# Performance work log

Hardware: AMD Instinct MI355X
Metric: run time of the kernel (lower is better)

Reference implementation:

```python
import jax
import jax.numpy as jnp
import numpy as np

IN_FEATS = 784
HIDDEN_DIM = 1024
BATCH = 1024


def setup_inputs() -> dict:
    key = jax.random.key(0)
    k_px, k_W, k_c, k_V, k_b = jax.random.split(key, 5)
    pixels = jax.random.uniform(k_px, (BATCH, IN_FEATS), dtype=jnp.float32)
    W = jax.random.normal(k_W, (HIDDEN_DIM, IN_FEATS), dtype=jnp.float32)
    c = jax.random.normal(k_c, (HIDDEN_DIM,), dtype=jnp.float32)
    V = jax.random.normal(k_V, (IN_FEATS, HIDDEN_DIM), dtype=jnp.float32)
    b = jax.random.normal(k_b, (IN_FEATS,), dtype=jnp.float32)
    return {"pixels": pixels, "W": W, "c": c, "V": V, "b": b}


def reference(pixels, W, c, V, b):
    # pixels: [B, D]; W: [H, D]; c: [H]; V: [D, H]; b: [D]
    B = pixels.shape[0]
    a0 = jnp.broadcast_to(c[None, :], (B, c.shape[0]))  # [B, H]

    def step(a, inp):
        w_col, v_row, b_i, x_i = inp  # [H], [H], [], [B]
        h = jax.nn.sigmoid(a)                     # [B, H]
        pred_i = b_i + h @ v_row                  # [B]
        a_next = a + w_col[None, :] * x_i[:, None]  # rank-1 accumulator update
        return a_next, pred_i

    xs = (W.T, V, b, pixels.T)  # each leading dim D (scan over visible units)
    _, preds = jax.lax.scan(step, a0, xs)  # preds: [D, B]
    return preds.T  # [B, D]
```

## Files before the change

### kernel.cpp

```cpp
#include <hip/hip_runtime.h>
#include <stdint.h>

#define B_ 1024
#define D_ 784
#define H_ 1024
#define BH_ (B_ * H_)
#define LOG2E 1.4426950408889634f


typedef float v2f __attribute__((ext_vector_type(2)));

__device__ __forceinline__ int seg_bound(int s) {
    const int b[5] = {0, 200, 392, 592, 784};
    return b[s];
}

__device__ __forceinline__ size_t vw_idx(int i, int h, int part) {
    return (size_t)i * 2048 + (part * 4 + ((h & 7) >> 1)) * 256
         + ((h & 511) >> 3) * 4 + (h & 1) * 2 + (h >> 9);
}

__global__ __launch_bounds__(256) void prep(const float* __restrict__ V,
                                            const float* __restrict__ W,
                                            const float* __restrict__ px,
                                            float* __restrict__ VWf,
                                            float* __restrict__ G) {
    __shared__ float smem[1056];
    const int t = threadIdx.x;

    if (blockIdx.x < 800) {
        int i0 = (blockIdx.x % 25) * 32;
        int h0 = (blockIdx.x / 25) * 32;
        int tx = t & 31, ty = t >> 5;
#pragma unroll
        for (int j = 0; j < 4; ++j) {
            int i = i0 + ty + j * 8;
            if (i < D_)
                VWf[vw_idx(i, h0 + tx, 0)] = V[(size_t)i * H_ + h0 + tx];
        }
#pragma unroll
        for (int j = 0; j < 4; ++j) {
            int h = h0 + ty + j * 8;
            int i = i0 + tx;
            float v = 0.f;
            if (i < D_) v = W[(size_t)h * D_ + i] * -LOG2E;
            smem[(ty + j * 8) * 33 + tx] = v;
        }
        __syncthreads();
#pragma unroll
        for (int j = 0; j < 4; ++j) {
            int i = i0 + ty + j * 8;
            if (i < D_)
                VWf[vw_idx(i, h0 + tx, 1)] = smem[tx * 33 + ty + j * 8];
        }
    } else {
        float* xs = smem;
        float* ws = smem + 512;
        int idx = blockIdx.x - 800;
        int r   = idx >> 8;
        int b0  = (idx & 15) * 64;
        int h0  = ((idx >> 4) & 15) * 64;
        int j0s = seg_bound(r), j1s = seg_bound(r + 1);

        const int tb = t >> 4, th = t & 15;
        float acc[4][4];
#pragma unroll
        for (int bi = 0; bi < 4; ++bi)
#pragma unroll
            for (int hh = 0; hh < 4; ++hh) acc[bi][hh] = 0.f;

        const int xb = t >> 3;
        const int xj = t & 7;
        const int wh = t >> 1, wj = (t & 1) * 4;

        for (int j0 = j0s; j0 < j1s; j0 += 8) {
            float xv0 = px[(size_t)(b0 + xb) * D_ + j0 + xj];
            float xv1 = px[(size_t)(b0 + 32 + xb) * D_ + j0 + xj];
            float4 wv = make_float4(0, 0, 0, 0);
            if (t < 128) wv = *(const float4*)(W + (size_t)(h0 + wh) * D_ + j0 + wj);
            __syncthreads();
            xs[xj * 64 + xb]      = xv0;
            xs[xj * 64 + 32 + xb] = xv1;
            if (t < 128) {
                ws[(wj + 0) * 64 + wh] = wv.x * LOG2E;
                ws[(wj + 1) * 64 + wh] = wv.y * LOG2E;
                ws[(wj + 2) * 64 + wh] = wv.z * LOG2E;
                ws[(wj + 3) * 64 + wh] = wv.w * LOG2E;
            }
            __syncthreads();
#pragma unroll
            for (int jj = 0; jj < 8; ++jj) {
                float4 xq = *(float4*)&xs[jj * 64 + tb * 4];
                float4 wq = *(float4*)&ws[jj * 64 + th * 4];
                float xa[4] = {xq.x, xq.y, xq.z, xq.w};
                float wa[4] = {wq.x, wq.y, wq.z, wq.w};
#pragma unroll
                for (int bi = 0; bi < 4; ++bi)
#pragma unroll
                    for (int hh = 0; hh < 4; ++hh)
                        acc[bi][hh] = fmaf(xa[bi], wa[hh], acc[bi][hh]);
            }
        }
        float* dst = G + (size_t)r * BH_;
#pragma unroll
        for (int bi = 0; bi < 4; ++bi) {
            float4 o = make_float4(acc[bi][0], acc[bi][1], acc[bi][2], acc[bi][3]);
            *(float4*)(dst + (size_t)(b0 + tb * 4 + bi) * H_ + h0 + th * 4) = o;
        }
    }
}

template <int CTRL>
__device__ __forceinline__ float dpp_add(float p) {
    int s = __builtin_amdgcn_update_dpp(0, __float_as_int(p), CTRL, 0xf, 0xf, true);
    return p + __int_as_float(s);
}
__device__ __forceinline__ float reduce64(float p) {
    p = dpp_add<0x111>(p);
    p = dpp_add<0x112>(p);
    p = dpp_add<0x114>(p);
    p = dpp_add<0x118>(p);
    p = dpp_add<0x142>(p);
    p = dpp_add<0x143>(p);
    return p;
}

__device__ __forceinline__ void tree16(v2f (&An)[8], const float4 (&Va)[4], const float4 (&Wa)[4],
                                       float xi, v2f& n, v2f& d) {
    const v2f* va = (const v2f*)&Va[0];
    const v2f* wa = (const v2f*)&Wa[0];
    const v2f one = {1.f, 1.f};
    const v2f clamp15 = {15.f, 15.f};
    v2f xiv; xiv.x = xi; xiv.y = xi;
    v2f q[8];
#pragma unroll
    for (int k = 0; k < 8; ++k) {
        v2f m = __builtin_elementwise_min(clamp15, An[k]);
        v2f e;
        e.x = __builtin_amdgcn_exp2f(m.x);
        e.y = __builtin_amdgcn_exp2f(m.y);
        q[k] = one + e;
        An[k] = wa[k] * xiv + An[k];
    }
    v2f a01 = va[0] * q[1] + va[1] * q[0];
    v2f a23 = va[2] * q[3] + va[3] * q[2];
    v2f a45 = va[4] * q[5] + va[5] * q[4];
    v2f a67 = va[6] * q[7] + va[7] * q[6];
    v2f q01 = q[0] * q[1], q23 = q[2] * q[3];
    v2f q45 = q[4] * q[5], q67 = q[6] * q[7];
    v2f n0123 = a01 * q23 + a23 * q01;
    v2f n4567 = a45 * q67 + a67 * q45;
    v2f q0123 = q01 * q23, q4567 = q45 * q67;
    d = q0123 * q4567;
    n = n0123 * q4567 + n4567 * q0123;
}

__global__ __launch_bounds__(256, 4) void nade_main(
    const float* __restrict__ px,
    const float* __restrict__ c,
    const float* __restrict__ VWf,
    const float* __restrict__ G,
    const float* __restrict__ bias,
    float* __restrict__ out)
{
    const int lane = threadIdx.x & 63;
    const int wid  = threadIdx.x >> 6;
    const int bid  = blockIdx.x;
    const int s    = (bid >> 1) & 3;
    const int rb   = ((bid >> 3) << 1) | (bid & 1);
    const int row  = rb * 4 + wid;

    const int i0s = seg_bound(s), i1s = seg_bound(s + 1);

    const int hA = lane * 8;
    const int hB = 512 + hA;

    v2f An[8];
    {
        float4 c0 = *(const float4*)(c + hA);
        float4 c1 = *(const float4*)(c + hA + 4);
        float4 c2 = *(const float4*)(c + hB);
        float4 c3 = *(const float4*)(c + hB + 4);
        An[0].x = -c0.x * LOG2E; An[0].y = -c2.x * LOG2E;
        An[1].x = -c0.y * LOG2E; An[1].y = -c2.y * LOG2E;
        An[2].x = -c0.z * LOG2E; An[2].y = -c2.z * LOG2E;
        An[3].x = -c0.w * LOG2E; An[3].y = -c2.w * LOG2E;
        An[4].x = -c1.x * LOG2E; An[4].y = -c3.x * LOG2E;
        An[5].x = -c1.y * LOG2E; An[5].y = -c3.y * LOG2E;
        An[6].x = -c1.z * LOG2E; An[6].y = -c3.z * LOG2E;
        An[7].x = -c1.w * LOG2E; An[7].y = -c3.w * LOG2E;
        for (int r = 0; r < s; ++r) {
            const float* gp = G + (size_t)r * BH_ + (size_t)row * H_;
            float4 g0 = *(const float4*)(gp + hA);
            float4 g1 = *(const float4*)(gp + hA + 4);
            float4 g2 = *(const float4*)(gp + hB);
            float4 g3 = *(const float4*)(gp + hB + 4);
            An[0].x -= g0.x; An[0].y -= g2.x;
            An[1].x -= g0.y; An[1].y -= g2.y;
            An[2].x -= g0.z; An[2].y -= g2.z;
            An[3].x -= g0.w; An[3].y -= g2.w;
            An[4].x -= g1.x; An[4].y -= g3.x;
            An[5].x -= g1.y; An[5].y -= g3.y;
            An[6].x -= g1.z; An[6].y -= g3.z;
            An[7].x -= g1.w; An[7].y -= g3.w;
        }
    }

    const float* xp = px + (size_t)row * D_;
    const float* vp = VWf + (size_t)i0s * 2048 + lane * 4;

    float4 VaC[4], WaC[4];
#pragma unroll
    for (int u = 0; u < 4; ++u) {
        VaC[u] = *(const float4*)(vp + u * 256);
        WaC[u] = *(const float4*)(vp + 1024 + u * 256);
    }
    vp += 2048;
    float4 xq = *(const float4*)(xp + i0s);

    for (int ib = i0s; ib < i1s; ib += 4) {
        int xb = (ib + 4 < i1s) ? (ib + 4) : i0s;
        float4 xq_n = *(const float4*)(xp + xb);
        float xa[4] = {xq.x, xq.y, xq.z, xq.w};
        float pr[4];
#pragma unroll
        for (int j = 0; j < 4; ++j) {
            float4 VaN[4], WaN[4];
#pragma unroll
            for (int u = 0; u < 4; ++u) {
                VaN[u] = *(const float4*)(vp + u * 256);
                WaN[u] = *(const float4*)(vp + 1024 + u * 256);
            }
            vp += 2048;
            v2f n, d;
            tree16(An, VaC, WaC, xa[j], n, d);
            float p = fmaf(n.x, __builtin_amdgcn_rcpf(d.x),
                           n.y * __builtin_amdgcn_rcpf(d.y));
            pr[j] = reduce64(p);
#pragma unroll
            for (int u = 0; u < 4; ++u) { VaC[u] = VaN[u]; WaC[u] = WaN[u]; }
        }
        float4 b4 = *(const float4*)(bias + ib);
        if (lane == 63) {
            float4 o = make_float4(pr[0] + b4.x, pr[1] + b4.y, pr[2] + b4.z, pr[3] + b4.w);
            *(float4*)(out + (size_t)row * D_ + ib) = o;
        }
        xq = xq_n;
    }
}

extern "C" void kernel_launch(void* const* d_in, const int* in_sizes, int n_in,
                              void* d_out, int out_size, void* d_ws, size_t ws_size,
                              hipStream_t stream) {
    const float* px   = (const float*)d_in[0];
    const float* W    = (const float*)d_in[1];
    const float* c    = (const float*)d_in[2];
    const float* V    = (const float*)d_in[3];
    const float* bias = (const float*)d_in[4];
    float* out = (float*)d_out;

    float* VWf = (float*)d_ws;
    float* G   = (float*)((char*)d_ws + (size_t)788 * 8192);

    prep<<<dim3(1568), 256, 0, stream>>>(V, W, px, VWf, G);

    nade_main<<<dim3(1024), 256, 0, stream>>>(px, c, VWf, G, bias, out);
}
```

Before: 317.9 us.

## Fuse prep and main kernels into one cooperative launch with grid sync

Merges the transpose/prep kernel and the partial-GEMM prep into the main NADE kernel. Prep work runs as a grid-stride task loop, followed by a cooperative grid-wide sync before the recurrence phase, which removes one kernel launch and the gap between kernels. The VWf transpose is also rewritten to stage both W and V tiles in shared memory and emit float4 stores. This adds 16.5KB of shared memory per block, which may limit occupancy at 4 blocks/CU, and it relies on a cooperative launch of 1024 blocks being co-resident. If that launch fails, it falls back to two launches.

```diff
diff --git a/kernel.cpp b/kernel.cpp
--- a/kernel.cpp
+++ b/kernel.cpp
@@ -1,5 +1,8 @@
 #include <hip/hip_runtime.h>
+#include <hip/hip_cooperative_groups.h>
 #include <stdint.h>
+
+namespace cg = cooperative_groups;
 
 #define B_ 1024
 #define D_ 784
@@ -13,101 +16,6 @@
 __device__ __forceinline__ int seg_bound(int s) {
     const int b[5] = {0, 200, 392, 592, 784};
     return b[s];
-}
-
-__device__ __forceinline__ size_t vw_idx(int i, int h, int part) {
-    return (size_t)i * 2048 + (part * 4 + ((h & 7) >> 1)) * 256
-         + ((h & 511) >> 3) * 4 + (h & 1) * 2 + (h >> 9);
-}
-
-__global__ __launch_bounds__(256) void prep(const float* __restrict__ V,
-                                            const float* __restrict__ W,
-                                            const float* __restrict__ px,
-                                            float* __restrict__ VWf,
-                                            float* __restrict__ G) {
-    __shared__ float smem[1056];
-    const int t = threadIdx.x;
-
-    if (blockIdx.x < 800) {
-        int i0 = (blockIdx.x % 25) * 32;
-        int h0 = (blockIdx.x / 25) * 32;
-        int tx = t & 31, ty = t >> 5;
-#pragma unroll
-        for (int j = 0; j < 4; ++j) {
-            int i = i0 + ty + j * 8;
-            if (i < D_)
-                VWf[vw_idx(i, h0 + tx, 0)] = V[(size_t)i * H_ + h0 + tx];
-        }
-#pragma unroll
-        for (int j = 0; j < 4; ++j) {
-            int h = h0 + ty + j * 8;
-            int i = i0 + tx;
-            float v = 0.f;
-            if (i < D_) v = W[(size_t)h * D_ + i] * -LOG2E;
-            smem[(ty + j * 8) * 33 + tx] = v;
-        }
-        __syncthreads();
-#pragma unroll
-        for (int j = 0; j < 4; ++j) {
-            int i = i0 + ty + j * 8;
-            if (i < D_)
-                VWf[vw_idx(i, h0 + tx, 1)] = smem[tx * 33 + ty + j * 8];
-        }
-    } else {
-        float* xs = smem;
-        float* ws = smem + 512;
-        int idx = blockIdx.x - 800;
-        int r   = idx >> 8;
-        int b0  = (idx & 15) * 64;
-        int h0  = ((idx >> 4) & 15) * 64;
-        int j0s = seg_bound(r), j1s = seg_bound(r + 1);
-
-        const int tb = t >> 4, th = t & 15;
-        float acc[4][4];
-#pragma unroll
-        for (int bi = 0; bi < 4; ++bi)
-#pragma unroll
-            for (int hh = 0; hh < 4; ++hh) acc[bi][hh] = 0.f;
-
-        const int xb = t >> 3;
-        const int xj = t & 7;
-        const int wh = t >> 1, wj = (t & 1) * 4;
-
-        for (int j0 = j0s; j0 < j1s; j0 += 8) {
-            float xv0 = px[(size_t)(b0 + xb) * D_ + j0 + xj];
-            float xv1 = px[(size_t)(b0 + 32 + xb) * D_ + j0 + xj];
-            float4 wv = make_float4(0, 0, 0, 0);
-            if (t < 128) wv = *(const float4*)(W + (size_t)(h0 + wh) * D_ + j0 + wj);
-            __syncthreads();
-            xs[xj * 64 + xb]      = xv0;
-            xs[xj * 64 + 32 + xb] = xv1;
-            if (t < 128) {
-                ws[(wj + 0) * 64 + wh] = wv.x * LOG2E;
-                ws[(wj + 1) * 64 + wh] = wv.y * LOG2E;
-                ws[(wj + 2) * 64 + wh] = wv.z * LOG2E;
-                ws[(wj + 3) * 64 + wh] = wv.w * LOG2E;
-            }
-            __syncthreads();
-#pragma unroll
-            for (int jj = 0; jj < 8; ++jj) {
-                float4 xq = *(float4*)&xs[jj * 64 + tb * 4];
-                float4 wq = *(float4*)&ws[jj * 64 + th * 4];
-                float xa[4] = {xq.x, xq.y, xq.z, xq.w};
-                float wa[4] = {wq.x, wq.y, wq.z, wq.w};
-#pragma unroll
-                for (int bi = 0; bi < 4; ++bi)
-#pragma unroll
-                    for (int hh = 0; hh < 4; ++hh)
-                        acc[bi][hh] = fmaf(xa[bi], wa[hh], acc[bi][hh]);
-            }
-        }
-        float* dst = G + (size_t)r * BH_;
-#pragma unroll
-        for (int bi = 0; bi < 4; ++bi) {
-            float4 o = make_float4(acc[bi][0], acc[bi][1], acc[bi][2], acc[bi][3]);
-            *(float4*)(dst + (size_t)(b0 + tb * 4 + bi) * H_ + h0 + th * 4) = o;
-        }
-    }
 }
 
 template <int CTRL>
@@ -155,97 +63,217 @@
     n = n0123 * q4567 + n4567 * q0123;
 }
 
-__global__ __launch_bounds__(256, 4) void nade_main(
+__global__ __launch_bounds__(256, 4) void nade_fused(
     const float* __restrict__ px,
+    const float* __restrict__ W,
     const float* __restrict__ c,
-    const float* __restrict__ VWf,
-    const float* __restrict__ G,
+    const float* __restrict__ V,
     const float* __restrict__ bias,
-    float* __restrict__ out)
+    float* __restrict__ VWf,
+    float* __restrict__ G,
+    float* __restrict__ out,
+    int mode)
 {
-    const int lane = threadIdx.x & 63;
-    const int wid  = threadIdx.x >> 6;
-    const int bid  = blockIdx.x;
-    const int s    = (bid >> 1) & 3;
-    const int rb   = ((bid >> 3) << 1) | (bid & 1);
-    const int row  = rb * 4 + wid;
-
-    const int i0s = seg_bound(s), i1s = seg_bound(s + 1);
-
-    const int hA = lane * 8;
-    const int hB = 512 + hA;
-
-    v2f An[8];
+    __shared__ float smem[4224];
+    const int t   = threadIdx.x;
+    const int bid = blockIdx.x;
+
+    if (mode != 1) {
+        for (int task = bid; task < 1168; task += gridDim.x) {
+            __syncthreads();
+            if (task < 768) {
+                float* xs = smem;
+                float* ws = smem + 512;
+                int idx = task;
+                int r   = idx >> 8;
+                int b0  = (idx & 15) * 64;
+                int h0  = ((idx >> 4) & 15) * 64;
+                int j0s = seg_bound(r), j1s = seg_bound(r + 1);
+
+                const int tb = t >> 4, th = t & 15;
+                float acc[4][4];
+#pragma unroll
+                for (int bi = 0; bi < 4; ++bi)
+#pragma unroll
+                    for (int hh = 0; hh < 4; ++hh) acc[bi][hh] = 0.f;
+
+                const int xb = t >> 3;
+                const int xj = t & 7;
+                const int wh = t >> 1, wj = (t & 1) * 4;
+
+                for (int j0 = j0s; j0 < j1s; j0 += 8) {
+                    float xv0 = px[(size_t)(b0 + xb) * D_ + j0 + xj];
+                    float xv1 = px[(size_t)(b0 + 32 + xb) * D_ + j0 + xj];
+                    float4 wv = make_float4(0, 0, 0, 0);
+                    if (t < 128) wv = *(const float4*)(W + (size_t)(h0 + wh) * D_ + j0 + wj);
+                    __syncthreads();
+                    xs[xj * 64 + xb]      = xv0;
+                    xs[xj * 64 + 32 + xb] = xv1;
+                    if (t < 128) {
+                        ws[(wj + 0) * 64 + wh] = wv.x * LOG2E;
+                        ws[(wj + 1) * 64 + wh] = wv.y * LOG2E;
+                        ws[(wj + 2) * 64 + wh] = wv.z * LOG2E;
+                        ws[(wj + 3) * 64 + wh] = wv.w * LOG2E;
+                    }
+                    __syncthreads();
+#pragma unroll
+                    for (int jj = 0; jj < 8; ++jj) {
+                        float4 xq = *(float4*)&xs[jj * 64 + tb * 4];
+                        float4 wq = *(float4*)&ws[jj * 64 + th * 4];
+                        float xa[4] = {xq.x, xq.y, xq.z, xq.w};
+                        float wa[4] = {wq.x, wq.y, wq.z, wq.w};
+#pragma unroll
+                        for (int bi = 0; bi < 4; ++bi)
+#pragma unroll
+                            for (int hh = 0; hh < 4; ++hh)
+                                acc[bi][hh] = fmaf(xa[bi], wa[hh], acc[bi][hh]);
+                    }
+                }
+                float* dst = G + (size_t)r * BH_;
+#pragma unroll
+                for (int bi = 0; bi < 4; ++bi) {
+                    float4 o = make_float4(acc[bi][0], acc[bi][1], acc[bi][2], acc[bi][3]);
+                    *(float4*)(dst + (size_t)(b0 + tb * 4 + bi) * H_ + h0 + th * 4) = o;
+                }
+            } else {
+                int pt = task - 768;
+                int i0 = (pt % 25) * 32;
+                int h0 = (pt / 25) * 32;
+                float* smW = smem;
+                float* smV = smem + 2112;
+                const int tx = t & 31, ty = t >> 5;
+#pragma unroll
+                for (int u = 0; u < 2; ++u)
+#pragma unroll
+                    for (int j = 0; j < 4; ++j) {
+                        int rl = ty + j * 8;
+                        float w = 0.f;
+                        int iw = i0 + tx;
+                        if (iw < D_) w = W[(size_t)(h0 + u * 512 + rl) * D_ + iw] * -LOG2E;
+                        smW[u * 1056 + rl * 33 + tx] = w;
+                        float v = 0.f;
+                        int iv = i0 + rl;
+                        if (iv < D_) v = V[(size_t)iv * H_ + h0 + u * 512 + tx];
+                        smV[u * 1056 + rl * 33 + tx] = v;
+                    }
+                __syncthreads();
+                const int img = t >> 3;
+                const int iw  = i0 + img;
+                if (iw < D_) {
+                    const int sub = t & 7;
+                    const int sp  = sub >> 1;
+                    const int q   = sub & 1;
+                    float vv[8], wv[8];
+#pragma unroll
+                    for (int e = 0; e < 8; ++e) {
+                        int p = q * 8 + e;
+                        int m = p >> 2, par = (p >> 1) & 1, comp = p & 1;
+                        int hl = 8 * m + sp * 2 + par;
+                        wv[e] = smW[comp * 1056 + hl * 33 + img];
+                        vv[e] = smV[comp * 1056 + img * 33 + hl];
+                    }
+                    float* dst = VWf + (size_t)iw * 2048;
+                    int cb = h0 / 2 + q * 8;
+                    *(float4*)(dst + sp * 256 + cb)           = make_float4(vv[0], vv[1], vv[2], vv[3]);
+                    *(float4*)(dst + sp * 256 + cb + 4)       = make_float4(vv[4], vv[5], vv[6], vv[7]);
+                    *(float4*)(dst + (4 + sp) * 256 + cb)     = make_float4(wv[0], wv[1], wv[2], wv[3]);
+                    *(float4*)(dst + (4 + sp) * 256 + cb + 4) = make_float4(wv[4], wv[5], wv[6], wv[7]);
+                }
+            }
+        }
+    }
+
+    if (mode == 2) {
+        __threadfence();
+        cg::this_grid().sync();
+        __threadfence();
+    }
+    if (mode == 0) return;
+
     {
-        float4 c0 = *(const float4*)(c + hA);
-        float4 c1 = *(const float4*)(c + hA + 4);
-        float4 c2 = *(const float4*)(c + hB);
-        float4 c3 = *(const float4*)(c + hB + 4);
-        An[0].x = -c0.x * LOG2E; An[0].y = -c2.x * LOG2E;
-        An[1].x = -c0.y * LOG2E; An[1].y = -c2.y * LOG2E;
-        An[2].x = -c0.z * LOG2E; An[2].y = -c2.z * LOG2E;
-        An[3].x = -c0.w * LOG2E; An[3].y = -c2.w * LOG2E;
-        An[4].x = -c1.x * LOG2E; An[4].y = -c3.x * LOG2E;
-        An[5].x = -c1.y * LOG2E; An[5].y = -c3.y * LOG2E;
-        An[6].x = -c1.z * LOG2E; An[6].y = -c3.z * LOG2E;
-        An[7].x = -c1.w * LOG2E; An[7].y = -c3.w * LOG2E;
-        for (int r = 0; r < s; ++r) {
-            const float* gp = G + (size_t)r * BH_ + (size_t)row * H_;
-            float4 g0 = *(const float4*)(gp + hA);
-            float4 g1 = *(const float4*)(gp + hA + 4);
-            float4 g2 = *(const float4*)(gp + hB);
-            float4 g3 = *(const float4*)(gp + hB + 4);
-            An[0].x -= g0.x; An[0].y -= g2.x;
-            An[1].x -= g0.y; An[1].y -= g2.y;
-            An[2].x -= g0.z; An[2].y -= g2.z;
-            An[3].x -= g0.w; An[3].y -= g2.w;
-            An[4].x -= g1.x; An[4].y -= g3.x;
-            An[5].x -= g1.y; An[5].y -= g3.y;
-            An[6].x -= g1.z; An[6].y -= g3.z;
-            An[7].x -= g1.w; An[7].y -= g3.w;
+        const int lane = t & 63;
+        const int wid  = t >> 6;
+        const int s    = (bid >> 1) & 3;
+        const int rb   = ((bid >> 3) << 1) | (bid & 1);
+        const int row  = rb * 4 + wid;
+
+        const int i0s = seg_bound(s), i1s = seg_bound(s + 1);
+
+        const int hA = lane * 8;
+        const int hB = 512 + hA;
+
+        v2f An[8];
+        {
+            float4 c0 = *(const float4*)(c + hA);
+            float4 c1 = *(const float4*)(c + hA + 4);
+            float4 c2 = *(const float4*)(c + hB);
+            float4 c3 = *(const float4*)(c + hB + 4);
+            An[0].x = -c0.x * LOG2E; An[0].y = -c2.x * LOG2E;
+            An[1].x = -c0.y * LOG2E; An[1].y = -c2.y * LOG2E;
+            An[2].x = -c0.z * LOG2E; An[2].y = -c2.z * LOG2E;
+            An[3].x = -c0.w * LOG2E; An[3].y = -c2.w * LOG2E;
+            An[4].x = -c1.x * LOG2E; An[4].y = -c3.x * LOG2E;
+            An[5].x = -c1.y * LOG2E; An[5].y = -c3.y * LOG2E;
+            An[6].x = -c1.z * LOG2E; An[6].y = -c3.z * LOG2E;
+            An[7].x = -c1.w * LOG2E; An[7].y = -c3.w * LOG2E;
+            for (int r = 0; r < s; ++r) {
+                const float* gp = G + (size_t)r * BH_ + (size_t)row * H_;
+                float4 g0 = *(const float4*)(gp + hA);
+                float4 g1 = *(const float4*)(gp + hA + 4);
+                float4 g2 = *(const float4*)(gp + hB);
+                float4 g3 = *(const float4*)(gp + hB + 4);
+                An[0].x -= g0.x; An[0].y -= g2.x;
+                An[1].x -= g0.y; An[1].y -= g2.y;
+                An[2].x -= g0.z; An[2].y -= g2.z;
+                An[3].x -= g0.w; An[3].y -= g2.w;
+                An[4].x -= g1.x; An[4].y -= g3.x;
+                An[5].x -= g1.y; An[5].y -= g3.y;
+                An[6].x -= g1.z; An[6].y -= g3.z;
+                An[7].x -= g1.w; An[7].y -= g3.w;
+            }
         }
-    }
-
-    const float* xp = px + (size_t)row * D_;
-    const float* vp = VWf + (size_t)i0s * 2048 + lane * 4;
-
-    float4 VaC[4], WaC[4];
-#pragma unroll
-    for (int u = 0; u < 4; ++u) {
-        VaC[u] = *(const float4*)(vp + u * 256);
-        WaC[u] = *(const float4*)(vp + 1024 + u * 256);
-    }
-    vp += 2048;
-    float4 xq = *(const float4*)(xp + i0s);
-
-    for (int ib = i0s; ib < i1s; ib += 4) {
-        int xb = (ib + 4 < i1s) ? (ib + 4) : i0s;
-        float4 xq_n = *(const float4*)(xp + xb);
-        float xa[4] = {xq.x, xq.y, xq.z, xq.w};
-        float pr[4];
-#pragma unroll
-        for (int j = 0; j < 4; ++j) {
-            float4 VaN[4], WaN[4];
-#pragma unroll
-            for (int u = 0; u < 4; ++u) {
-                VaN[u] = *(const float4*)(vp + u * 256);
-                WaN[u] = *(const float4*)(vp + 1024 + u * 256);
+
+        const float* xp = px + (size_t)row * D_;
+        const float* vp = VWf + (size_t)i0s * 2048 + lane * 4;
+
+        float4 VaC[4], WaC[4];
+#pragma unroll
+        for (int u = 0; u < 4; ++u) {
+            VaC[u] = *(const float4*)(vp + u * 256);
+            WaC[u] = *(const float4*)(vp + 1024 + u * 256);
+        }
+        vp += 2048;
+        float4 xq = *(const float4*)(xp + i0s);
+
+        for (int ib = i0s; ib < i1s; ib += 4) {
+            int xb = (ib + 4 < i1s) ? (ib + 4) : i0s;
+            float4 xq_n = *(const float4*)(xp + xb);
+            float xa[4] = {xq.x, xq.y, xq.z, xq.w};
+            float pr[4];
+#pragma unroll
+            for (int j = 0; j < 4; ++j) {
+                float4 VaN[4], WaN[4];
+#pragma unroll
+                for (int u = 0; u < 4; ++u) {
+                    VaN[u] = *(const float4*)(vp + u * 256);
+                    WaN[u] = *(const float4*)(vp + 1024 + u * 256);
+                }
+                vp += 2048;
+                v2f n, d;
+                tree16(An, VaC, WaC, xa[j], n, d);
+                float p = fmaf(n.x, __builtin_amdgcn_rcpf(d.x),
+                               n.y * __builtin_amdgcn_rcpf(d.y));
+                pr[j] = reduce64(p);
+#pragma unroll
+                for (int u = 0; u < 4; ++u) { VaC[u] = VaN[u]; WaC[u] = WaN[u]; }
             }
-            vp += 2048;
-            v2f n, d;
-            tree16(An, VaC, WaC, xa[j], n, d);
-            float p = fmaf(n.x, __builtin_amdgcn_rcpf(d.x),
-                           n.y * __builtin_amdgcn_rcpf(d.y));
-            pr[j] = reduce64(p);
-#pragma unroll
-            for (int u = 0; u < 4; ++u) { VaC[u] = VaN[u]; WaC[u] = WaN[u]; }
+            float4 b4 = *(const float4*)(bias + ib);
+            if (lane == 63) {
+                float4 o = make_float4(pr[0] + b4.x, pr[1] + b4.y, pr[2] + b4.z, pr[3] + b4.w);
+                *(float4*)(out + (size_t)row * D_ + ib) = o;
+            }
+            xq = xq_n;
         }
-        float4 b4 = *(const float4*)(bias + ib);
-        if (lane == 63) {
-            float4 o = make_float4(pr[0] + b4.x, pr[1] + b4.y, pr[2] + b4.z, pr[3] + b4.w);
-            *(float4*)(out + (size_t)row * D_ + ib) = o;
-        }
-        xq = xq_n;
     }
 }
 
@@ -262,7 +290,14 @@
     float* VWf = (float*)d_ws;
     float* G   = (float*)((char*)d_ws + (size_t)788 * 8192);
 
-    prep<<<dim3(1568), 256, 0, stream>>>(V, W, px, VWf, G);
-
-    nade_main<<<dim3(1024), 256, 0, stream>>>(px, c, VWf, G, bias, out);
-}
+    int mode = 2;
+    void* args[9] = {(void*)&px, (void*)&W, (void*)&c, (void*)&V, (void*)&bias,
+                     (void*)&VWf, (void*)&G, (void*)&out, (void*)&mode};
+    hipError_t err = hipLaunchCooperativeKernel(nade_fused, dim3(1024), dim3(256),
+                                                args, 0u, stream);
+    if (err != hipSuccess) {
+        (void)hipGetLastError();
+        nade_fused<<<dim3(1168), 256, 0, stream>>>(px, W, c, V, bias, VWf, G, out, 0);
+        nade_fused<<<dim3(1024), 256, 0, stream>>>(px, W, c, V, bias, VWf, G, out, 1);
+    }
+}
```

New measurement: 620.0 us. 1.95x slower.
